# Kernel optimization log

Measured on AMD Instinct MI355X. Metric: run time of the kernel, lower is better.

## Reference

```python
import jax, jax.numpy as jnp
import numpy as np

N_USER = 100000
N_ITEM = 50000
N = N_USER + N_ITEM  # 150000 nodes
D = 64               # embedding_size
L = 3                # num_layers
E = 2000000          # edges
B = 8192             # batch of (user, item_p, item_n) triples
INT_W, POP_W, TIDE_W = 0.1, 0.1, 0.2


def setup_inputs() -> dict:
    key = jax.random.key(0)
    ks = jax.random.split(key, 10)
    stdv = 1.0 / np.sqrt(D)
    emb_int = jax.random.uniform(ks[0], (N, D), minval=-stdv, maxval=stdv, dtype=jnp.float32)
    emb_pop = jax.random.uniform(ks[1], (N, D), minval=-stdv, maxval=stdv, dtype=jnp.float32)
    q = jax.random.uniform(ks[2], (N_ITEM,), dtype=jnp.float32)
    b = jax.random.uniform(ks[3], (N_ITEM,), dtype=jnp.float32)
    user = jax.random.randint(ks[4], (B, 1), 0, N_USER)
    item_p = jax.random.randint(ks[5], (B, 1), 0, N_ITEM)
    item_n = jax.random.randint(ks[6], (B, 1), 0, N_ITEM)
    mask = jax.random.randint(ks[7], (B, 1), 0, 2).astype(bool)
    edge_src = jax.random.randint(ks[8], (E,), 0, N)
    edge_dst = jax.random.randint(ks[9], (E,), 0, N)
    return {"emb_int": emb_int, "emb_pop": emb_pop, "q": q, "b": b,
            "user": user, "item_p": item_p, "item_n": item_n, "mask": mask,
            "edge_src": edge_src, "edge_dst": edge_dst}


def reference(emb_int, emb_pop, q, b, user, item_p, item_n, mask, edge_src, edge_dst):
    # --- LightGCN symmetric normalization coefficients (per edge) ---
    ones = jnp.ones(edge_src.shape, emb_int.dtype)
    deg_out = jax.ops.segment_sum(ones, edge_src, num_segments=N)
    deg_in = jax.ops.segment_sum(ones, edge_dst, num_segments=N)
    norm = (jax.lax.rsqrt(jnp.maximum(deg_out, 1.0))[edge_src]
            * jax.lax.rsqrt(jnp.maximum(deg_in, 1.0))[edge_dst])  # [E]

    def propagate(e0):
        # L layers of LGConv (gather-scale-scatter), mean over layer outputs incl. layer 0.
        # Dropout is identity in eval mode (training=False).
        acc, h = e0, e0
        for _ in range(L):
            h = jax.ops.segment_sum(h[edge_src] * norm[:, None], edge_dst, num_segments=N)
            acc = acc + h
        return acc / (L + 1)

    f_int = propagate(emb_int)  # [N, D]
    f_pop = propagate(emb_pop)  # [N, D]

    ip = item_p + N_USER  # item node ids
    inn = item_n + N_USER
    u_i, u_p = f_int[user], f_pop[user]          # [B, 1, D]
    pi_i, pi_p = f_int[ip], f_pop[ip]
    ni_i, ni_p = f_int[inn], f_pop[inn]

    p_score_int = jnp.sum(u_i * pi_i, axis=2)    # [B, 1]
    n_score_int = jnp.sum(u_i * ni_i, axis=2)
    p_score_pop = jnp.sum(u_p * pi_p, axis=2)
    n_score_pop = jnp.sum(u_p * ni_p, axis=2)
    p_score_total = p_score_int + p_score_pop
    n_score_total = n_score_int + n_score_pop

    mf = mask.astype(p_score_int.dtype)
    nmf = (~mask).astype(p_score_int.dtype)

    def mask_bpr(p, n, m):
        return -jnp.mean(m * jax.nn.log_sigmoid(p - n))

    def bpr(p, n):
        return -jnp.mean(jax.nn.log_sigmoid(p - n))

    loss_int = mask_bpr(p_score_int, n_score_int, mf)
    loss_pop = mask_bpr(n_score_pop, p_score_pop, mf) - mask_bpr(p_score_pop, n_score_pop, nmf)

    pop_p = jax.nn.softplus(q[item_p]) + jax.nn.softplus(b[item_p])  # [B, 1]
    pop_n = jax.nn.softplus(q[item_n]) + jax.nn.softplus(b[item_n])
    loss_tide = bpr(jnp.tanh(pop_p) * p_score_total, jnp.tanh(pop_n) * n_score_total)

    return INT_W * loss_int + POP_W * loss_pop + TIDE_W * loss_tide
```

## Files before the change

### kernel.cpp

```cpp
#include <hip/hip_runtime.h>
#include <hip/hip_bf16.h>
#include <math.h>

#define N_USER 100000
#define N_ITEM 50000
#define NNODE  150000
#define DIM    64
#define NEDGE  2000000
#define BSZ    8192
#define NTGT   (3*BSZ)
#define CB     586
#define NB     512
#define CH     ((NEDGE + NB - 1)/NB)
#define LBLK   2048
#define PREPB  (NNODE*32/256)
#define CAP    5120

#ifndef __has_builtin
#define __has_builtin(x) 0
#endif
#if __has_builtin(__builtin_amdgcn_make_buffer_rsrc) && __has_builtin(__builtin_amdgcn_raw_buffer_load_b32)
#define USE_BUF 1
#else
#define USE_BUF 0
#endif

typedef float v2f __attribute__((ext_vector_type(2)));

__device__ __forceinline__ float logsigf(float x){
    return fminf(x, 0.f) - log1pf(expf(-fabsf(x)));
}
__device__ __forceinline__ float softplusf(float x){
    return fmaxf(x, 0.f) + log1pf(expf(-fabsf(x)));
}
__device__ __forceinline__ v2f fp8x2_to_f32(unsigned short u){
    return __builtin_amdgcn_cvt_pk_f32_fp8((int)u, false);
}
__device__ __forceinline__ unsigned short f32_to_fp8x2(float a, float b){
    return (unsigned short)__builtin_amdgcn_cvt_pk_fp8_f32(a, b, 0, false);
}
__device__ __forceinline__ unsigned rfl(unsigned v){
    return (unsigned)__builtin_amdgcn_readfirstlane((int)v);
}
__device__ __forceinline__ unsigned umax2(unsigned a, unsigned b){ return a>b ? a : b; }

#if USE_BUF
typedef __amdgpu_buffer_rsrc_t rsrc_t;
__device__ __forceinline__ rsrc_t mkrsrc(const unsigned* p, unsigned bytes){
    return __builtin_amdgcn_make_buffer_rsrc((void*)p, (short)0, (int)bytes, 0x00020000);
}
__device__ __forceinline__ unsigned bload(rsrc_t r, int voff, int soff){
    return (unsigned)__builtin_amdgcn_raw_buffer_load_b32(r, voff, soff, 0);
}
#define DEF_ROW(J) rsrc_t R##J = mkrsrc(ec + s##J, c##J*4u);
#define LOADE(J,K,i) bload(R##J, 4*(K), (int)(4u*(i)))
#else
#define DEF_ROW(J)
#define LOADE(J,K,i) ((((i)+(K)) < c##J) ? __builtin_nontemporal_load(&ec[s##J + (i) + (K)]) : 0u)
#endif

__device__ __forceinline__ void scanCB(unsigned* arr, unsigned* tmp){
    int t = threadIdx.x;
    int base = 3*t;
    unsigned a0=0,a1=0,a2=0;
    if(base   < CB) a0 = arr[base];
    if(base+1 < CB) a1 = arr[base+1];
    if(base+2 < CB) a2 = arr[base+2];
    unsigned s = a0+a1+a2;
    tmp[t]=s; __syncthreads();
    for(int off=1; off<256; off<<=1){
        unsigned v = (t>=off)? tmp[t-off] : 0u;
        __syncthreads();
        tmp[t] += v;
        __syncthreads();
    }
    unsigned excl = tmp[t]-s;
    if(base   < CB) arr[base]   = excl;
    if(base+1 < CB) arr[base+1] = excl+a0;
    if(base+2 < CB) arr[base+2] = excl+a0+a1;
    __syncthreads();
}

__global__ __launch_bounds__(256) void k_hist(const int* __restrict__ src, const int* __restrict__ dst,
                       unsigned* __restrict__ histD, unsigned* __restrict__ histS,
                       const unsigned char* __restrict__ mask8, unsigned* __restrict__ mflag){
    if(blockIdx.x == NB){
        __shared__ int any;
        if(threadIdx.x==0) any=0;
        __syncthreads();
        for(int i=threadIdx.x;i<BSZ;i+=256){ if((i&3) && mask8[i]) any=1; }
        __syncthreads();
        if(threadIdx.x==0) *mflag = (any!=0) ? 1u : 0u;
        return;
    }
    __shared__ unsigned hD[CB], hS[CB];
    for(int i=threadIdx.x;i<CB;i+=256){ hD[i]=0; hS[i]=0; }
    __syncthreads();
    int lo = blockIdx.x*CH, hi = min(lo+CH, NEDGE);
    for(int e=lo+threadIdx.x; e<hi; e+=256){
        atomicAdd(&hS[src[e]>>8],1u);
        atomicAdd(&hD[dst[e]>>8],1u);
    }
    __syncthreads();
    for(int i=threadIdx.x;i<CB;i+=256){
        histD[(size_t)blockIdx.x*CB + i]=hD[i];
        histS[(size_t)blockIdx.x*CB + i]=hS[i];
    }
}

__global__ __launch_bounds__(512) void k_colscan(unsigned* __restrict__ histD, unsigned* __restrict__ histS,
                          unsigned* __restrict__ ctD, unsigned* __restrict__ ctS){
    unsigned* hist = blockIdx.y ? histS : histD;
    unsigned* ct   = blockIdx.y ? ctS   : ctD;
    int b = blockIdx.x;
    __shared__ unsigned sh[512];
    unsigned v = hist[(size_t)threadIdx.x*CB + b];
    sh[threadIdx.x] = v;
    __syncthreads();
    for(int off=1; off<512; off<<=1){
        unsigned t = (threadIdx.x>=off)? sh[threadIdx.x-off] : 0u;
        __syncthreads();
        sh[threadIdx.x] += t;
        __syncthreads();
    }
    hist[(size_t)threadIdx.x*CB + b] = sh[threadIdx.x] - v;
    if(threadIdx.x==511) ct[b] = sh[511];
}

__global__ __launch_bounds__(1024) void k_bstart(const unsigned* __restrict__ ctD, const unsigned* __restrict__ ctS,
                         unsigned* __restrict__ bsD, unsigned* __restrict__ bsS){
    __shared__ unsigned sh[1024];
    unsigned v = (threadIdx.x<CB)? ctD[threadIdx.x] : 0u;
    sh[threadIdx.x]=v; __syncthreads();
    for(int off=1; off<1024; off<<=1){ unsigned t=(threadIdx.x>=off)?sh[threadIdx.x-off]:0u; __syncthreads(); sh[threadIdx.x]+=t; __syncthreads(); }
    if(threadIdx.x<CB) bsD[threadIdx.x]=sh[threadIdx.x]-v;
    if(threadIdx.x==CB-1) bsD[CB]=sh[threadIdx.x];
    __syncthreads();
    unsigned v2 = (threadIdx.x<CB)? ctS[threadIdx.x] : 0u;
    sh[threadIdx.x]=v2; __syncthreads();
    for(int off=1; off<1024; off<<=1){ unsigned t=(threadIdx.x>=off)?sh[threadIdx.x-off]:0u; __syncthreads(); sh[threadIdx.x]+=t; __syncthreads(); }
    if(threadIdx.x<CB) bsS[threadIdx.x]=sh[threadIdx.x]-v2;
    if(threadIdx.x==CB-1) bsS[CB]=sh[threadIdx.x];
}

__global__ __launch_bounds__(256) void k_scatter(const int* __restrict__ src, const int* __restrict__ dst,
                          const unsigned* __restrict__ histD, const unsigned* __restrict__ histS,
                          const unsigned* __restrict__ bsD, const unsigned* __restrict__ bsS,
                          unsigned* __restrict__ part, unsigned char* __restrict__ spart){
    __shared__ unsigned curD[CB], curS[CB];
    __shared__ unsigned lhD[CB], lhS[CB];
    __shared__ unsigned startD[CB], startS[CB];
    __shared__ unsigned tmp[256];
    __shared__ unsigned partl[CH];
    __shared__ unsigned short keyD[CH];
    __shared__ unsigned short keyS[CH];
    __shared__ unsigned char sl[CH];
    for(int i=threadIdx.x;i<CB;i+=256){
        curD[i]=bsD[i]+histD[(size_t)blockIdx.x*CB+i];
        curS[i]=bsS[i]+histS[(size_t)blockIdx.x*CB+i];
        lhD[i]=0; lhS[i]=0;
    }
    __syncthreads();
    int lo=blockIdx.x*CH, hi=min(lo+CH,NEDGE);
    int n = hi-lo;
    for(int e=lo+threadIdx.x;e<hi;e+=256){
        atomicAdd(&lhD[dst[e]>>8],1u);
        atomicAdd(&lhS[src[e]>>8],1u);
    }
    __syncthreads();
    scanCB(lhD, tmp);
    scanCB(lhS, tmp);
    for(int i=threadIdx.x;i<CB;i+=256){ startD[i]=lhD[i]; startS[i]=lhS[i]; }
    __syncthreads();
    for(int e=lo+threadIdx.x;e<hi;e+=256){
        int s=src[e], d=dst[e];
        unsigned bd=(unsigned)(d>>8);
        unsigned slot=atomicAdd(&lhD[bd],1u);
        partl[slot]=((unsigned)(d&255)<<18)|(unsigned)s;
        keyD[slot]=(unsigned short)bd;
        unsigned bs=(unsigned)(s>>8);
        unsigned sslot=atomicAdd(&lhS[bs],1u);
        sl[sslot]=(unsigned char)(s&255);
        keyS[sslot]=(unsigned short)bs;
    }
    __syncthreads();
    for(int k=threadIdx.x;k<n;k+=256){
        unsigned b=keyD[k];
        part[curD[b] + (unsigned)k - startD[b]] = partl[k];
    }
    for(int k=threadIdx.x;k<n;k+=256){
        unsigned b=keyS[k];
        spart[curS[b] + (unsigned)k - startS[b]] = sl[k];
    }
}

__global__ __launch_bounds__(256) void k_degO(const unsigned char* __restrict__ spart, const unsigned* __restrict__ bsS,
                       float* __restrict__ rsqO, float* __restrict__ sqd){
    __shared__ unsigned cnt[256];
    cnt[threadIdx.x]=0;
    __syncthreads();
    unsigned lo=bsS[blockIdx.x], hi=bsS[blockIdx.x+1];
    for(unsigned e=lo+threadIdx.x;e<hi;e+=256) atomicAdd(&cnt[spart[e]],1u);
    __syncthreads();
    int node=(blockIdx.x<<8)+(int)threadIdx.x;
    if(node<NNODE){
        float dv = fmaxf((float)cnt[threadIdx.x],1.f);
        rsqO[node]=rsqrtf(dv);
        sqd[node]=sqrtf(dv)*0.125f;
    }
}

__global__ __launch_bounds__(256) void k_prep(const float2* __restrict__ ei, const float2* __restrict__ ep,
                      const float* __restrict__ rsqO,
                      unsigned* __restrict__ hE32, unsigned* __restrict__ h1g, unsigned* __restrict__ h2g,
                      unsigned* __restrict__ ecpad){
    if(blockIdx.x == PREPB){
        int t = threadIdx.x;
        if(t < 32) hE32[t] = 0u;
        else if(t < 64) h1g[t-32] = 0u;
        else if(t < 96) h2g[t-64] = 0u;
        else if(t < 160) ecpad[t-96] = 0u;
        return;
    }
    int idx = blockIdx.x*256 + threadIdx.x;
    int n = idx>>5, c = idx&31;
    float sc = 8.f*rsqO[n];
    float2 va, vb;
    if(c<16){ va = ei[(size_t)n*32 + 2*c]; vb = ei[(size_t)n*32 + 2*c+1]; }
    else    { va = ep[(size_t)n*32 + 2*c-32]; vb = ep[(size_t)n*32 + 2*c-31]; }
    int d = __builtin_amdgcn_cvt_pk_fp8_f32(va.x*sc, va.y*sc, 0, false);
    d = __builtin_amdgcn_cvt_pk_fp8_f32(vb.x*sc, vb.y*sc, d, true);
    hE32[32 + (size_t)n*32 + c] = (unsigned)d;
}

__global__ __launch_bounds__(256) void k_csr(const unsigned* __restrict__ part, const unsigned* __restrict__ bsD,
                      const float* __restrict__ rsqO,
                      unsigned* __restrict__ rs, unsigned* __restrict__ degI,
                      unsigned* __restrict__ ec, float* __restrict__ srow, float* __restrict__ rsqI8){
    __shared__ unsigned cnt[256], cur[256], sh[256];
    __shared__ unsigned partl[CAP];
    cnt[threadIdx.x]=0;
    __syncthreads();
    unsigned lo=bsD[blockIdx.x], hi=bsD[blockIdx.x+1];
    unsigned n = hi-lo;
    for(unsigned e=lo+threadIdx.x;e<hi;e+=256) atomicAdd(&cnt[part[e]>>18],1u);
    __syncthreads();
    unsigned c=cnt[threadIdx.x];
    sh[threadIdx.x]=c; __syncthreads();
    for(int o=1;o<256;o<<=1){ unsigned t=(threadIdx.x>=o)?sh[threadIdx.x-o]:0u; __syncthreads(); sh[threadIdx.x]+=t; __syncthreads(); }
    unsigned ex = sh[threadIdx.x]-c;
    cur[threadIdx.x]=ex;
    int node=(blockIdx.x<<8)+(int)threadIdx.x;
    if(node<NNODE){
        degI[node]=c; rs[node]=lo+ex;
        float rI = rsqrtf(fmaxf((float)c,1.f));
        float rO = rsqO[node];
        srow[node]  = rI*rO;
        rsqI8[node] = rI*0.125f;
    }
    __syncthreads();
    if(n <= CAP){
        for(unsigned e=lo+threadIdx.x;e<hi;e+=256){
            unsigned p=part[e];
            unsigned slot=atomicAdd(&cur[p>>18],1u);
            partl[slot]=p;
        }
        __syncthreads();
        for(unsigned k=threadIdx.x;k<n;k+=256){
            unsigned p=partl[k];
            ec[lo+k] = ((p&0x3FFFFu)+1u)<<7;
        }
    } else {
        for(unsigned e=lo+threadIdx.x;e<hi;e+=256){
            unsigned p=part[e];
            unsigned pos=lo+atomicAdd(&cur[p>>18],1u);
            ec[pos] = ((p&0x3FFFFu)+1u)<<7;
        }
    }
}

__global__ __launch_bounds__(256) void k_spmm_c(const unsigned short* __restrict__ hinb, unsigned short* __restrict__ houtb,
                                                const unsigned* __restrict__ rs, const unsigned* __restrict__ degI,
                                                const unsigned* __restrict__ ec, const float* __restrict__ srow){
    int wv = (blockIdx.x*256 + threadIdx.x) >> 6;
    int lane = threadIdx.x & 63;
    int r = 4*wv;
    if(r >= NNODE) return;
    unsigned s0=rfl(rs[r  ]), c0=rfl(degI[r  ]);
    unsigned s1=rfl(rs[r+1]), c1=rfl(degI[r+1]);
    unsigned s2=rfl(rs[r+2]), c2=rfl(degI[r+2]);
    unsigned s3=rfl(rs[r+3]), c3=rfl(degI[r+3]);
    DEF_ROW(0) DEF_ROW(1) DEF_ROW(2) DEF_ROW(3)
    const char* hb = (const char*)hinb;
    unsigned lane2 = ((unsigned)lane)*2u;
    v2f a0={0.f,0.f}, a1={0.f,0.f}, a2={0.f,0.f}, a3={0.f,0.f};
    unsigned cmax = umax2(umax2(c0,c1), umax2(c2,c3));
    for(unsigned i=0; i<cmax; i+=4){
        unsigned eA0=LOADE(0,0,i), eA1=LOADE(0,1,i), eA2=LOADE(0,2,i), eA3=LOADE(0,3,i);
        unsigned eB0=LOADE(1,0,i), eB1=LOADE(1,1,i), eB2=LOADE(1,2,i), eB3=LOADE(1,3,i);
        unsigned eC0=LOADE(2,0,i), eC1=LOADE(2,1,i), eC2=LOADE(2,2,i), eC3=LOADE(2,3,i);
        unsigned eD0=LOADE(3,0,i), eD1=LOADE(3,1,i), eD2=LOADE(3,2,i), eD3=LOADE(3,3,i);
        unsigned short uA0=*(const unsigned short*)(hb+eA0+lane2);
        unsigned short uA1=*(const unsigned short*)(hb+eA1+lane2);
        unsigned short uA2=*(const unsigned short*)(hb+eA2+lane2);
        unsigned short uA3=*(const unsigned short*)(hb+eA3+lane2);
        unsigned short uB0=*(const unsigned short*)(hb+eB0+lane2);
        unsigned short uB1=*(const unsigned short*)(hb+eB1+lane2);
        unsigned short uB2=*(const unsigned short*)(hb+eB2+lane2);
        unsigned short uB3=*(const unsigned short*)(hb+eB3+lane2);
        unsigned short uC0=*(const unsigned short*)(hb+eC0+lane2);
        unsigned short uC1=*(const unsigned short*)(hb+eC1+lane2);
        unsigned short uC2=*(const unsigned short*)(hb+eC2+lane2);
        unsigned short uC3=*(const unsigned short*)(hb+eC3+lane2);
        unsigned short uD0=*(const unsigned short*)(hb+eD0+lane2);
        unsigned short uD1=*(const unsigned short*)(hb+eD1+lane2);
        unsigned short uD2=*(const unsigned short*)(hb+eD2+lane2);
        unsigned short uD3=*(const unsigned short*)(hb+eD3+lane2);
        a0 += fp8x2_to_f32(uA0); a0 += fp8x2_to_f32(uA1); a0 += fp8x2_to_f32(uA2); a0 += fp8x2_to_f32(uA3);
        a1 += fp8x2_to_f32(uB0); a1 += fp8x2_to_f32(uB1); a1 += fp8x2_to_f32(uB2); a1 += fp8x2_to_f32(uB3);
        a2 += fp8x2_to_f32(uC0); a2 += fp8x2_to_f32(uC1); a2 += fp8x2_to_f32(uC2); a2 += fp8x2_to_f32(uC3);
        a3 += fp8x2_to_f32(uD0); a3 += fp8x2_to_f32(uD1); a3 += fp8x2_to_f32(uD2); a3 += fp8x2_to_f32(uD3);
    }
    float sc0=srow[r], sc1=srow[r+1], sc2=srow[r+2], sc3=srow[r+3];
    houtb[(size_t)(r+1)*64+lane] = f32_to_fp8x2(sc0*a0.x, sc0*a0.y);
    houtb[(size_t)(r+2)*64+lane] = f32_to_fp8x2(sc1*a1.x, sc1*a1.y);
    houtb[(size_t)(r+3)*64+lane] = f32_to_fp8x2(sc2*a2.x, sc2*a2.y);
    houtb[(size_t)(r+4)*64+lane] = f32_to_fp8x2(sc3*a3.x, sc3*a3.y);
}

__global__ __launch_bounds__(256) void k_spmm_t(const unsigned short* __restrict__ hinb, float2* __restrict__ h3,
                                                const unsigned* __restrict__ rs, const unsigned* __restrict__ degI,
                                                const unsigned* __restrict__ ec, const float* __restrict__ rsqI8,
                                                const int* __restrict__ user, const int* __restrict__ itp,
                                                const int* __restrict__ itn){
    int wv = (blockIdx.x*256 + threadIdx.x) >> 6;
    int lane = threadIdx.x & 63;
    int t0 = 2*wv, t1 = 2*wv+1;
    if(t0 >= NTGT) return;
    int sec0 = t0>>13, b0 = t0&(BSZ-1);
    int sec1 = t1>>13, b1 = t1&(BSZ-1);
    int n0 = (sec0==0) ? user[b0] : ((sec0==1) ? itp[b0]+N_USER : itn[b0]+N_USER);
    int n1 = (sec1==0) ? user[b1] : ((sec1==1) ? itp[b1]+N_USER : itn[b1]+N_USER);
    n0 = __builtin_amdgcn_readfirstlane(n0);
    n1 = __builtin_amdgcn_readfirstlane(n1);
    unsigned s0 = rfl(rs[n0]), c0 = rfl(degI[n0]);
    unsigned s1 = rfl(rs[n1]), c1 = rfl(degI[n1]);
    DEF_ROW(0) DEF_ROW(1)
    const char* hb = (const char*)hinb;
    unsigned lane2 = ((unsigned)lane)*2u;
    v2f a0={0.f,0.f}, a1={0.f,0.f};
    unsigned cmax = umax2(c0,c1);
    for(unsigned i=0; i<cmax; i+=4){
        unsigned eA0=LOADE(0,0,i), eA1=LOADE(0,1,i), eA2=LOADE(0,2,i), eA3=LOADE(0,3,i);
        unsigned eB0=LOADE(1,0,i), eB1=LOADE(1,1,i), eB2=LOADE(1,2,i), eB3=LOADE(1,3,i);
        unsigned short uA0=*(const unsigned short*)(hb+eA0+lane2);
        unsigned short uA1=*(const unsigned short*)(hb+eA1+lane2);
        unsigned short uA2=*(const unsigned short*)(hb+eA2+lane2);
        unsigned short uA3=*(const unsigned short*)(hb+eA3+lane2);
        unsigned short uB0=*(const unsigned short*)(hb+eB0+lane2);
        unsigned short uB1=*(const unsigned short*)(hb+eB1+lane2);
        unsigned short uB2=*(const unsigned short*)(hb+eB2+lane2);
        unsigned short uB3=*(const unsigned short*)(hb+eB3+lane2);
        a0 += fp8x2_to_f32(uA0); a0 += fp8x2_to_f32(uA1); a0 += fp8x2_to_f32(uA2); a0 += fp8x2_to_f32(uA3);
        a1 += fp8x2_to_f32(uB0); a1 += fp8x2_to_f32(uB1); a1 += fp8x2_to_f32(uB2); a1 += fp8x2_to_f32(uB3);
    }
    float t0s = rsqI8[n0], t1s = rsqI8[n1];
    h3[(size_t)t0*64+lane] = make_float2(a0.x*t0s, a0.y*t0s);
    h3[(size_t)t1*64+lane] = make_float2(a1.x*t1s, a1.y*t1s);
}

__global__ __launch_bounds__(256) void k_scoreloss(const float2* __restrict__ ei, const float2* __restrict__ ep,
                        const unsigned short* __restrict__ h1C, const unsigned short* __restrict__ h2C,
                        const float2* __restrict__ h3,
                        const float* __restrict__ q, const float* __restrict__ bq,
                        const int* __restrict__ user, const int* __restrict__ item_p, const int* __restrict__ item_n,
                        const void* __restrict__ mask, const unsigned* __restrict__ mflag,
                        const float* __restrict__ sqd,
                        float4* __restrict__ partial){
    int t = blockIdx.x*256 + threadIdx.x;
    int b = t >> 6, l = t & 63;
    int wv = threadIdx.x >> 6;
    __shared__ float4 wsum[4];
    int nu = user[b];
    int np = item_p[b] + N_USER;
    int nn = item_n[b] + N_USER;

    float2 e0u, e0p, e0n;
    if(l < 32){
        e0u = ei[(size_t)nu*32 + l]; e0p = ei[(size_t)np*32 + l]; e0n = ei[(size_t)nn*32 + l];
    } else {
        e0u = ep[(size_t)nu*32 + (l-32)]; e0p = ep[(size_t)np*32 + (l-32)]; e0n = ep[(size_t)nn*32 + (l-32)];
    }
    v2f h1u = fp8x2_to_f32(h1C[(size_t)(nu+1)*64 + l]);
    v2f h1p = fp8x2_to_f32(h1C[(size_t)(np+1)*64 + l]);
    v2f h1n = fp8x2_to_f32(h1C[(size_t)(nn+1)*64 + l]);
    v2f h2u = fp8x2_to_f32(h2C[(size_t)(nu+1)*64 + l]);
    v2f h2p = fp8x2_to_f32(h2C[(size_t)(np+1)*64 + l]);
    v2f h2n = fp8x2_to_f32(h2C[(size_t)(nn+1)*64 + l]);
    float2 h3u = h3[(size_t)b*64 + l];
    float2 h3p = h3[(size_t)(BSZ   + b)*64 + l];
    float2 h3n = h3[(size_t)(2*BSZ + b)*64 + l];

    float squ = sqd[nu], sqp = sqd[np], sqn = sqd[nn];

    float fux = e0u.x + squ*(h1u.x + h2u.x) + h3u.x, fuy = e0u.y + squ*(h1u.y + h2u.y) + h3u.y;
    float fpx = e0p.x + sqp*(h1p.x + h2p.x) + h3p.x, fpy = e0p.y + sqp*(h1p.y + h2p.y) + h3p.y;
    float fnx = e0n.x + sqn*(h1n.x + h2n.x) + h3n.x, fny = e0n.y + sqn*(h1n.y + h2n.y) + h3n.y;

    float dp = fux*fpx + fuy*fpy;
    float dn = fux*fnx + fuy*fny;
    for(int off=16; off; off>>=1){ dp += __shfl_down(dp,off,32); dn += __shfl_down(dn,off,32); }
    float pi  = __shfl(dp, 0, 64) * (1.f/16.f);
    float ni  = __shfl(dn, 0, 64) * (1.f/16.f);
    float pp  = __shfl(dp, 32, 64) * (1.f/16.f);
    float npp = __shfl(dn, 32, 64) * (1.f/16.f);
    if(l == 0){
        bool bytes = (*mflag)!=0;
        float mf = bytes ? (((const unsigned char*)mask)[b]?1.f:0.f)
                         : (((const int*)mask)[b]?1.f:0.f);
        float nmf = 1.f-mf;
        float a0 = mf  * logsigf(pi-ni);
        float a1 = mf  * logsigf(npp-pp);
        float a2 = nmf * logsigf(pp-npp);
        int ip=item_p[b], in_=item_n[b];
        float popp = softplusf(q[ip]) + softplusf(bq[ip]);
        float popn = softplusf(q[in_]) + softplusf(bq[in_]);
        float a3 = logsigf(tanhf(popp)*(pi+pp) - tanhf(popn)*(ni+npp));
        wsum[wv] = make_float4(a0,a1,a2,a3);
    }
    __syncthreads();
    if(threadIdx.x == 0){
        float4 s0=wsum[0], s1=wsum[1], s2=wsum[2], s3=wsum[3];
        partial[blockIdx.x] = make_float4(s0.x+s1.x+s2.x+s3.x, s0.y+s1.y+s2.y+s3.y,
                                          s0.z+s1.z+s2.z+s3.z, s0.w+s1.w+s2.w+s3.w);
    }
}

__global__ __launch_bounds__(256) void k_lossfin(const float4* __restrict__ partial, float* __restrict__ out){
    __shared__ float4 sh[256];
    float4 s = make_float4(0,0,0,0);
    for(int i=threadIdx.x; i<LBLK; i+=256){
        float4 v = partial[i];
        s.x+=v.x; s.y+=v.y; s.z+=v.z; s.w+=v.w;
    }
    sh[threadIdx.x]=s;
    __syncthreads();
    for(int off=128; off; off>>=1){
        if(threadIdx.x < off){
            float4 a=sh[threadIdx.x], b2=sh[threadIdx.x+off];
            sh[threadIdx.x]=make_float4(a.x+b2.x,a.y+b2.y,a.z+b2.z,a.w+b2.w);
        }
        __syncthreads();
    }
    if(threadIdx.x==0){
        const float invB = 1.f/(float)BSZ;
        float4 t = sh[0];
        float loss_int  = -t.x*invB;
        float loss_pop  = -t.y*invB + t.z*invB;
        float loss_tide = -t.w*invB;
        out[0] = 0.1f*loss_int + 0.1f*loss_pop + 0.2f*loss_tide;
    }
}

extern "C" void kernel_launch(void* const* d_in, const int* in_sizes, int n_in,
                              void* d_out, int out_size, void* d_ws, size_t ws_size,
                              hipStream_t stream){
    const float* emb_int = (const float*)d_in[0];
    const float* emb_pop = (const float*)d_in[1];
    const float* q    = (const float*)d_in[2];
    const float* bq   = (const float*)d_in[3];
    const int* user   = (const int*)d_in[4];
    const int* item_p = (const int*)d_in[5];
    const int* item_n = (const int*)d_in[6];
    const void* mask  = d_in[7];
    const int* esrc   = (const int*)d_in[8];
    const int* edst   = (const int*)d_in[9];

    char* ws = (char*)d_ws;
    size_t o = 0;
    auto take = [&](size_t bytes)->char*{ char* p = ws + o; o = (o + bytes + 255) & ~(size_t)255; return p; };
    unsigned* histD = (unsigned*)take((size_t)NB*CB*4);
    unsigned* histS = (unsigned*)take((size_t)NB*CB*4);
    unsigned* ctD   = (unsigned*)take((size_t)CB*4);
    unsigned* ctS   = (unsigned*)take((size_t)CB*4);
    unsigned* bsD   = (unsigned*)take((size_t)(CB+1)*4);
    unsigned* bsS   = (unsigned*)take((size_t)(CB+1)*4);
    unsigned* part  = (unsigned*)take((size_t)NEDGE*4);
    unsigned char* spart = (unsigned char*)take((size_t)NEDGE);
    float*    rsqO  = (float*)take((size_t)NNODE*4);
    float*    sqd   = (float*)take((size_t)NNODE*4);
    unsigned* rs    = (unsigned*)take((size_t)NNODE*4);
    unsigned* degI  = (unsigned*)take((size_t)NNODE*4);
    unsigned* ec    = (unsigned*)take((size_t)NEDGE*4 + 256);
    float*    srow  = (float*)take((size_t)NNODE*4);
    float*    rsqI8 = (float*)take((size_t)NNODE*4);
    unsigned short* hEb  = (unsigned short*)take((size_t)(NNODE+1)*64*2);
    unsigned short* h1Cb = (unsigned short*)take((size_t)(NNODE+1)*64*2);
    unsigned short* h2Cb = (unsigned short*)take((size_t)(NNODE+1)*64*2);
    float2*   h3    = (float2*)take((size_t)NTGT*64*8);
    float4*   partial = (float4*)take((size_t)LBLK*16);
    unsigned* mflag = (unsigned*)take(256);
    (void)ws_size; (void)in_sizes; (void)n_in; (void)out_size;

    k_hist<<<NB+1,256,0,stream>>>(esrc, edst, histD, histS,
                                  (const unsigned char*)mask, mflag);
    k_colscan<<<dim3(CB,2),512,0,stream>>>(histD, histS, ctD, ctS);
    k_bstart<<<1,1024,0,stream>>>(ctD, ctS, bsD, bsS);
    k_scatter<<<NB,256,0,stream>>>(esrc, edst, histD, histS, bsD, bsS, part, spart);
    k_degO<<<CB,256,0,stream>>>(spart, bsS, rsqO, sqd);
    k_csr<<<CB,256,0,stream>>>(part, bsD, rsqO, rs, degI, ec, srow, rsqI8);
    k_prep<<<PREPB+1,256,0,stream>>>((const float2*)emb_int, (const float2*)emb_pop, rsqO,
                                     (unsigned*)hEb, (unsigned*)h1Cb, (unsigned*)h2Cb,
                                     ec + NEDGE);

    const int spB = ((NNODE/4)*64 + 255)/256;
    k_spmm_c<<<spB,256,0,stream>>>(hEb,  h1Cb, rs, degI, ec, srow);
    k_spmm_c<<<spB,256,0,stream>>>(h1Cb, h2Cb, rs, degI, ec, srow);
    k_spmm_t<<<((NTGT/2)*64 + 255)/256,256,0,stream>>>(h2Cb, h3, rs, degI, ec, rsqI8,
                                                 user, item_p, item_n);
    k_scoreloss<<<LBLK,256,0,stream>>>((const float2*)emb_int, (const float2*)emb_pop,
                                       h1Cb, h2Cb, h3, q, bq, user, item_p, item_n,
                                       mask, mflag, sqd, partial);
    k_lossfin<<<1,256,0,stream>>>(partial, (float*)d_out);
}
```

Measured before the change: 360.2 us.

## Use one wavefront per row with half-wave edge split and 4-byte gathers

The SpMM kernels previously gave each wavefront four rows (two in the target kernel), with each lane gathering 2 bytes of fp8 per edge and the loop running to the longest of those rows. Now each wavefront handles a single row. The two half-waves process different edges, each lane gathers a 4-byte dword of 4 fp8 values, and the halves are combined with a cross-half shuffle before lanes 0-31 store. This is meant to remove wasted iterations on shorter rows and to widen each gather. In exchange it launches four times (two times) as many waves, and half the lanes sit idle during the final store.

New measurement: 396.6 us. 10.1% more time.

```diff
diff --git a/kernel.cpp b/kernel.cpp
--- a/kernel.cpp
+++ b/kernel.cpp
@@ -36,27 +36,23 @@
 __device__ __forceinline__ v2f fp8x2_to_f32(unsigned short u){
     return __builtin_amdgcn_cvt_pk_f32_fp8((int)u, false);
 }
-__device__ __forceinline__ unsigned short f32_to_fp8x2(float a, float b){
-    return (unsigned short)__builtin_amdgcn_cvt_pk_fp8_f32(a, b, 0, false);
-}
 __device__ __forceinline__ unsigned rfl(unsigned v){
     return (unsigned)__builtin_amdgcn_readfirstlane((int)v);
 }
-__device__ __forceinline__ unsigned umax2(unsigned a, unsigned b){ return a>b ? a : b; }
 
 #if USE_BUF
 typedef __amdgpu_buffer_rsrc_t rsrc_t;
 __device__ __forceinline__ rsrc_t mkrsrc(const unsigned* p, unsigned bytes){
     return __builtin_amdgcn_make_buffer_rsrc((void*)p, (short)0, (int)bytes, 0x00020000);
 }
-__device__ __forceinline__ unsigned bload(rsrc_t r, int voff, int soff){
-    return (unsigned)__builtin_amdgcn_raw_buffer_load_b32(r, voff, soff, 0);
+__device__ __forceinline__ unsigned bload(rsrc_t r, int voff){
+    return (unsigned)__builtin_amdgcn_raw_buffer_load_b32(r, voff, 0, 0);
 }
 #define DEF_ROW(J) rsrc_t R##J = mkrsrc(ec + s##J, c##J*4u);
-#define LOADE(J,K,i) bload(R##J, 4*(K), (int)(4u*(i)))
+#define LOADE(J,idx) bload(R##J, (int)(4u*(idx)))
 #else
 #define DEF_ROW(J)
-#define LOADE(J,K,i) ((((i)+(K)) < c##J) ? __builtin_nontemporal_load(&ec[s##J + (i) + (K)]) : 0u)
+#define LOADE(J,idx) (((idx) < c##J) ? __builtin_nontemporal_load(&ec[s##J + (idx)]) : 0u)
 #endif
 
 __device__ __forceinline__ void scanCB(unsigned* arr, unsigned* tmp){
@@ -284,48 +280,34 @@
                                                 const unsigned* __restrict__ ec, const float* __restrict__ srow){
     int wv = (blockIdx.x*256 + threadIdx.x) >> 6;
     int lane = threadIdx.x & 63;
-    int r = 4*wv;
-    if(r >= NNODE) return;
-    unsigned s0=rfl(rs[r  ]), c0=rfl(degI[r  ]);
-    unsigned s1=rfl(rs[r+1]), c1=rfl(degI[r+1]);
-    unsigned s2=rfl(rs[r+2]), c2=rfl(degI[r+2]);
-    unsigned s3=rfl(rs[r+3]), c3=rfl(degI[r+3]);
-    DEF_ROW(0) DEF_ROW(1) DEF_ROW(2) DEF_ROW(3)
+    if(wv >= NNODE) return;
+    int r = wv;
+    unsigned s0 = rfl(rs[r]), c0 = rfl(degI[r]);
+    DEF_ROW(0)
     const char* hb = (const char*)hinb;
-    unsigned lane2 = ((unsigned)lane)*2u;
-    v2f a0={0.f,0.f}, a1={0.f,0.f}, a2={0.f,0.f}, a3={0.f,0.f};
-    unsigned cmax = umax2(umax2(c0,c1), umax2(c2,c3));
-    for(unsigned i=0; i<cmax; i+=4){
-        unsigned eA0=LOADE(0,0,i), eA1=LOADE(0,1,i), eA2=LOADE(0,2,i), eA3=LOADE(0,3,i);
-        unsigned eB0=LOADE(1,0,i), eB1=LOADE(1,1,i), eB2=LOADE(1,2,i), eB3=LOADE(1,3,i);
-        unsigned eC0=LOADE(2,0,i), eC1=LOADE(2,1,i), eC2=LOADE(2,2,i), eC3=LOADE(2,3,i);
-        unsigned eD0=LOADE(3,0,i), eD1=LOADE(3,1,i), eD2=LOADE(3,2,i), eD3=LOADE(3,3,i);
-        unsigned short uA0=*(const unsigned short*)(hb+eA0+lane2);
-        unsigned short uA1=*(const unsigned short*)(hb+eA1+lane2);
-        unsigned short uA2=*(const unsigned short*)(hb+eA2+lane2);
-        unsigned short uA3=*(const unsigned short*)(hb+eA3+lane2);
-        unsigned short uB0=*(const unsigned short*)(hb+eB0+lane2);
-        unsigned short uB1=*(const unsigned short*)(hb+eB1+lane2);
-        unsigned short uB2=*(const unsigned short*)(hb+eB2+lane2);
-        unsigned short uB3=*(const unsigned short*)(hb+eB3+lane2);
-        unsigned short uC0=*(const unsigned short*)(hb+eC0+lane2);
-        unsigned short uC1=*(const unsigned short*)(hb+eC1+lane2);
-        unsigned short uC2=*(const unsigned short*)(hb+eC2+lane2);
-        unsigned short uC3=*(const unsigned short*)(hb+eC3+lane2);
-        unsigned short uD0=*(const unsigned short*)(hb+eD0+lane2);
-        unsigned short uD1=*(const unsigned short*)(hb+eD1+lane2);
-        unsigned short uD2=*(const unsigned short*)(hb+eD2+lane2);
-        unsigned short uD3=*(const unsigned short*)(hb+eD3+lane2);
-        a0 += fp8x2_to_f32(uA0); a0 += fp8x2_to_f32(uA1); a0 += fp8x2_to_f32(uA2); a0 += fp8x2_to_f32(uA3);
-        a1 += fp8x2_to_f32(uB0); a1 += fp8x2_to_f32(uB1); a1 += fp8x2_to_f32(uB2); a1 += fp8x2_to_f32(uB3);
-        a2 += fp8x2_to_f32(uC0); a2 += fp8x2_to_f32(uC1); a2 += fp8x2_to_f32(uC2); a2 += fp8x2_to_f32(uC3);
-        a3 += fp8x2_to_f32(uD0); a3 += fp8x2_to_f32(uD1); a3 += fp8x2_to_f32(uD2); a3 += fp8x2_to_f32(uD3);
-    }
-    float sc0=srow[r], sc1=srow[r+1], sc2=srow[r+2], sc3=srow[r+3];
-    houtb[(size_t)(r+1)*64+lane] = f32_to_fp8x2(sc0*a0.x, sc0*a0.y);
-    houtb[(size_t)(r+2)*64+lane] = f32_to_fp8x2(sc1*a1.x, sc1*a1.y);
-    houtb[(size_t)(r+3)*64+lane] = f32_to_fp8x2(sc2*a2.x, sc2*a2.y);
-    houtb[(size_t)(r+4)*64+lane] = f32_to_fp8x2(sc3*a3.x, sc3*a3.y);
+    unsigned h   = (unsigned)(lane >> 5);
+    unsigned dw4 = ((unsigned)(lane & 31))*4u;
+    v2f aL={0.f,0.f}, aH={0.f,0.f}, bL={0.f,0.f}, bH={0.f,0.f};
+    for(unsigned i=0; i<c0; i+=4){
+        unsigned eA = LOADE(0, i+h);
+        unsigned eB = LOADE(0, i+2u+h);
+        unsigned dA = *(const unsigned*)(hb + eA + dw4);
+        unsigned dB = *(const unsigned*)(hb + eB + dw4);
+        aL += __builtin_amdgcn_cvt_pk_f32_fp8((int)dA, false);
+        aH += __builtin_amdgcn_cvt_pk_f32_fp8((int)dA, true);
+        bL += __builtin_amdgcn_cvt_pk_f32_fp8((int)dB, false);
+        bH += __builtin_amdgcn_cvt_pk_f32_fp8((int)dB, true);
+    }
+    v2f sL = aL + bL, sH = aH + bH;
+    sL.x += __shfl_xor(sL.x, 32);
+    sL.y += __shfl_xor(sL.y, 32);
+    sH.x += __shfl_xor(sH.x, 32);
+    sH.y += __shfl_xor(sH.y, 32);
+    float sc = srow[r];
+    int d = __builtin_amdgcn_cvt_pk_fp8_f32(sc*sL.x, sc*sL.y, 0, false);
+    d = __builtin_amdgcn_cvt_pk_fp8_f32(sc*sH.x, sc*sH.y, d, true);
+    if(lane < 32)
+        ((unsigned*)houtb)[(size_t)(r+1)*32 + (lane & 31)] = (unsigned)d;
 }
 
 __global__ __launch_bounds__(256) void k_spmm_t(const unsigned short* __restrict__ hinb, float2* __restrict__ h3,
@@ -335,38 +317,37 @@
                                                 const int* __restrict__ itn){
     int wv = (blockIdx.x*256 + threadIdx.x) >> 6;
     int lane = threadIdx.x & 63;
-    int t0 = 2*wv, t1 = 2*wv+1;
-    if(t0 >= NTGT) return;
-    int sec0 = t0>>13, b0 = t0&(BSZ-1);
-    int sec1 = t1>>13, b1 = t1&(BSZ-1);
-    int n0 = (sec0==0) ? user[b0] : ((sec0==1) ? itp[b0]+N_USER : itn[b0]+N_USER);
-    int n1 = (sec1==0) ? user[b1] : ((sec1==1) ? itp[b1]+N_USER : itn[b1]+N_USER);
+    if(wv >= NTGT) return;
+    int t = wv;
+    int sec = t>>13, b = t&(BSZ-1);
+    int n0 = (sec==0) ? user[b] : ((sec==1) ? itp[b]+N_USER : itn[b]+N_USER);
     n0 = __builtin_amdgcn_readfirstlane(n0);
-    n1 = __builtin_amdgcn_readfirstlane(n1);
     unsigned s0 = rfl(rs[n0]), c0 = rfl(degI[n0]);
-    unsigned s1 = rfl(rs[n1]), c1 = rfl(degI[n1]);
-    DEF_ROW(0) DEF_ROW(1)
+    DEF_ROW(0)
     const char* hb = (const char*)hinb;
-    unsigned lane2 = ((unsigned)lane)*2u;
-    v2f a0={0.f,0.f}, a1={0.f,0.f};
-    unsigned cmax = umax2(c0,c1);
-    for(unsigned i=0; i<cmax; i+=4){
-        unsigned eA0=LOADE(0,0,i), eA1=LOADE(0,1,i), eA2=LOADE(0,2,i), eA3=LOADE(0,3,i);
-        unsigned eB0=LOADE(1,0,i), eB1=LOADE(1,1,i), eB2=LOADE(1,2,i), eB3=LOADE(1,3,i);
-        unsigned short uA0=*(const unsigned short*)(hb+eA0+lane2);
-        unsigned short uA1=*(const unsigned short*)(hb+eA1+lane2);
-        unsigned short uA2=*(const unsigned short*)(hb+eA2+lane2);
-        unsigned short uA3=*(const unsigned short*)(hb+eA3+lane2);
-        unsigned short uB0=*(const unsigned short*)(hb+eB0+lane2);
-        unsigned short uB1=*(const unsigned short*)(hb+eB1+lane2);
-        unsigned short uB2=*(const unsigned short*)(hb+eB2+lane2);
-        unsigned short uB3=*(const unsigned short*)(hb+eB3+lane2);
-        a0 += fp8x2_to_f32(uA0); a0 += fp8x2_to_f32(uA1); a0 += fp8x2_to_f32(uA2); a0 += fp8x2_to_f32(uA3);
-        a1 += fp8x2_to_f32(uB0); a1 += fp8x2_to_f32(uB1); a1 += fp8x2_to_f32(uB2); a1 += fp8x2_to_f32(uB3);
-    }
-    float t0s = rsqI8[n0], t1s = rsqI8[n1];
-    h3[(size_t)t0*64+lane] = make_float2(a0.x*t0s, a0.y*t0s);
-    h3[(size_t)t1*64+lane] = make_float2(a1.x*t1s, a1.y*t1s);
+    unsigned h   = (unsigned)(lane >> 5);
+    unsigned dw4 = ((unsigned)(lane & 31))*4u;
+    v2f aL={0.f,0.f}, aH={0.f,0.f}, bL={0.f,0.f}, bH={0.f,0.f};
+    for(unsigned i=0; i<c0; i+=4){
+        unsigned eA = LOADE(0, i+h);
+        unsigned eB = LOADE(0, i+2u+h);
+        unsigned dA = *(const unsigned*)(hb + eA + dw4);
+        unsigned dB = *(const unsigned*)(hb + eB + dw4);
+        aL += __builtin_amdgcn_cvt_pk_f32_fp8((int)dA, false);
+        aH += __builtin_amdgcn_cvt_pk_f32_fp8((int)dA, true);
+        bL += __builtin_amdgcn_cvt_pk_f32_fp8((int)dB, false);
+        bH += __builtin_amdgcn_cvt_pk_f32_fp8((int)dB, true);
+    }
+    v2f sL = aL + bL, sH = aH + bH;
+    sL.x += __shfl_xor(sL.x, 32);
+    sL.y += __shfl_xor(sL.y, 32);
+    sH.x += __shfl_xor(sH.x, 32);
+    sH.y += __shfl_xor(sH.y, 32);
+    float ts = rsqI8[n0];
+    if(lane < 32){
+        float4 o = make_float4(ts*sL.x, ts*sL.y, ts*sH.x, ts*sH.y);
+        ((float4*)h3)[(size_t)t*32 + (lane & 31)] = o;
+    }
 }
 
 __global__ __launch_bounds__(256) void k_scoreloss(const float2* __restrict__ ei, const float2* __restrict__ ep,
@@ -513,10 +494,10 @@
                                      (unsigned*)hEb, (unsigned*)h1Cb, (unsigned*)h2Cb,
                                      ec + NEDGE);
 
-    const int spB = ((NNODE/4)*64 + 255)/256;
+    const int spB = (NNODE*64)/256;
     k_spmm_c<<<spB,256,0,stream>>>(hEb,  h1Cb, rs, degI, ec, srow);
     k_spmm_c<<<spB,256,0,stream>>>(h1Cb, h2Cb, rs, degI, ec, srow);
-    k_spmm_t<<<((NTGT/2)*64 + 255)/256,256,0,stream>>>(h2Cb, h3, rs, degI, ec, rsqI8,
+    k_spmm_t<<<(NTGT*64)/256,256,0,stream>>>(h2Cb, h3, rs, degI, ec, rsqI8,
                                                  user, item_p, item_n);
     k_scoreloss<<<LBLK,256,0,stream>>>((const float2*)emb_int, (const float2*)emb_pop,
                                        h1Cb, h2Cb, h3, q, bq, user, item_p, item_n,
```
